# Kernel tuning notes

Measured on AMD Instinct MI355X. Metric: run time of the kernel, lower is better.

The kernel has to match this reference:

```python
import jax, jax.numpy as jnp
import numpy as np
from functools import partial

# dims
BATCH, L, H = 1, 512, 2048
NH, HD = 64, 64            # num heads, head dim
INTER = NH * HD            # 4096
G, N = 4, 64               # n_groups, ssm state size
K = 4                      # conv kernel
CONV = INTER + 2 * G * N   # 4608
PROJ = INTER + CONV + NH   # z, xBC, dt
EPS = 1e-5


def rmsnorm(x, w, eps=EPS):
    xf = x.astype(jnp.float32)
    v = jnp.mean(xf * xf, axis=-1, keepdims=True)
    return (xf * jax.lax.rsqrt(v + eps)).astype(x.dtype) * w


def setup_inputs() -> dict:
    key = jax.random.key(0)
    ks = jax.random.split(key, 12)
    rn = lambda k, s, sc=1.0: sc * jax.random.normal(k, s, dtype=jnp.float32)
    return {
        "hidden_states": rn(ks[0], (BATCH, L, H)),
        "residual": rn(ks[1], (BATCH, L, H)),
        "norm_w": 1.0 + rn(ks[2], (H,), 0.02),
        "in_proj_w": rn(ks[3], (H, PROJ), 0.02),
        "conv_w": rn(ks[4], (CONV, K), 0.2),
        "conv_b": rn(ks[5], (CONV,), 0.02),
        "A_log": jnp.log(jax.random.uniform(ks[6], (NH,), minval=1.0, maxval=16.0)),
        "dt_bias": rn(ks[7], (NH,), 0.5),
        "D": rn(ks[8], (NH,), 0.5),
        "gn_w": 1.0 + rn(ks[9], (INTER,), 0.02),
        "out_proj_w": rn(ks[10], (INTER, H), 0.02),
    }


def reference(hidden_states, residual, norm_w, in_proj_w, conv_w, conv_b,
              A_log, dt_bias, D, gn_w, out_proj_w):
    B_ = hidden_states.shape[0]
    # fused add + RMSNorm (residual is not None path)
    x = hidden_states + residual
    new_residual = x
    hs = rmsnorm(x, norm_w)

    # in_proj: [B,L,H] -> [B,L,PROJ] split into z | xBC | dt
    proj = jnp.einsum('blh,hp->blp', hs, in_proj_w)
    z = proj[..., :INTER]
    xBC = proj[..., INTER:INTER + CONV]
    dt = proj[..., INTER + CONV:]

    # causal depthwise conv of width K, then SiLU
    xp = jnp.pad(xBC, ((0, 0), (K - 1, 0), (0, 0)))
    conv = sum(xp[:, k:k + L, :] * conv_w[None, None, :, k] for k in range(K))
    xBC = jax.nn.silu(conv + conv_b)

    xh = xBC[..., :INTER].reshape(B_, L, NH, HD)
    Bm = xBC[..., INTER:INTER + G * N].reshape(B_, L, G, N)
    Cm = xBC[..., INTER + G * N:].reshape(B_, L, G, N)

    dt = jax.nn.softplus(dt + dt_bias)          # [B,L,NH]
    A = -jnp.exp(A_log)                         # [NH]
    dA = jnp.exp(dt * A)                        # [B,L,NH]

    hpg = NH // G
    Bh = jnp.repeat(Bm, hpg, axis=2)            # [B,L,NH,N]
    Ch = jnp.repeat(Cm, hpg, axis=2)

    def step(h, inp):
        dA_t, dt_t, x_t, B_t, C_t = inp
        # h: [B,NH,HD,N]
        h = h * dA_t[:, :, None, None] + (dt_t[:, :, None] * x_t)[..., None] * B_t[:, :, None, :]
        y = jnp.einsum('bhdn,bhn->bhd', h, C_t)
        return h, y

    h0 = jnp.zeros((B_, NH, HD, N), dtype=jnp.float32)
    xs = (jnp.moveaxis(dA, 1, 0), jnp.moveaxis(dt, 1, 0), jnp.moveaxis(xh, 1, 0),
          jnp.moveaxis(Bh, 1, 0), jnp.moveaxis(Ch, 1, 0))
    _, ys = jax.lax.scan(step, h0, xs)          # [L,B,NH,HD]
    y = jnp.moveaxis(ys, 0, 1) + xh * D[None, None, :, None]
    y = y.reshape(B_, L, INTER)

    # gated RMSNorm then out_proj
    y = rmsnorm(y * jax.nn.silu(z), gn_w)
    out = jnp.einsum('bli,ih->blh', y, out_proj_w)
    return out, new_residual
```

## Files before the change

kernel.cpp:

```cpp
#include <hip/hip_runtime.h>
#include <stdint.h>

#define LSEQ 512
#define HDIM 2048
#define NH 64
#define HD 64
#define INTER 4096
#define NG 4
#define NSTATE 64
#define CONVC 4608
#define PROJC 8768
#define EPS 1e-5f
#define CL 64
#define NC 8
#define NHDN (NH * HD * NSTATE)

typedef __attribute__((ext_vector_type(8))) short bf16x8;
typedef __attribute__((ext_vector_type(4))) short short4v;
typedef __attribute__((ext_vector_type(4))) float f32x4;

__device__ __forceinline__ short f2bf(float f) {
  union { float f; uint32_t u; } v; v.f = f;
  uint32_t r = v.u + 0x7FFFu + ((v.u >> 16) & 1u);
  return (short)(r >> 16);
}

__device__ __forceinline__ uint32_t cvt_pk_bf16(float lo, float hi) {
  uint32_t r;
  asm("v_cvt_pk_bf16_f32 %0, %1, %2" : "=v"(r) : "v"(lo), "v"(hi));
  return r;
}

__device__ __forceinline__ float bf2f(short s) {
  union { uint32_t u; float f; } v; v.u = ((uint32_t)(uint16_t)s) << 16;
  return v.f;
}

__device__ __forceinline__ float siluf(float v) {
  return v / (1.f + expf(-v));
}

__device__ __forceinline__ int xcd_swizzle(int orig, int nwg) {
  int q = nwg >> 3, r = nwg & 7;
  int xcd = orig & 7, idx = orig >> 3;
  return (xcd < r ? xcd * (q + 1) : r * (q + 1) + (xcd - r) * q) + idx;
}

__global__ __launch_bounds__(256) void k_add_rmsnorm(
    const float* __restrict__ hid, const float* __restrict__ res,
    const float* __restrict__ w, float* __restrict__ resid_out,
    short* __restrict__ hsb) {
  __shared__ float sred[4];
  const int row = blockIdx.x, tid = threadIdx.x;
  const float4* h4 = (const float4*)(hid + (size_t)row * HDIM);
  const float4* r4 = (const float4*)(res + (size_t)row * HDIM);
  float4* ro4 = (float4*)(resid_out + (size_t)row * HDIM);
  float4 a0 = h4[tid], b0 = r4[tid];
  float4 a1 = h4[tid + 256], b1 = r4[tid + 256];
  float4 xa, xb;
  xa.x = a0.x + b0.x; xa.y = a0.y + b0.y; xa.z = a0.z + b0.z; xa.w = a0.w + b0.w;
  xb.x = a1.x + b1.x; xb.y = a1.y + b1.y; xb.z = a1.z + b1.z; xb.w = a1.w + b1.w;
  ro4[tid] = xa; ro4[tid + 256] = xb;
  float ss = xa.x*xa.x + xa.y*xa.y + xa.z*xa.z + xa.w*xa.w
           + xb.x*xb.x + xb.y*xb.y + xb.z*xb.z + xb.w*xb.w;
  #pragma unroll
  for (int off = 32; off >= 1; off >>= 1) ss += __shfl_down(ss, off);
  if ((tid & 63) == 0) sred[tid >> 6] = ss;
  __syncthreads();
  float tot = sred[0] + sred[1] + sred[2] + sred[3];
  float rs = rsqrtf(tot / (float)HDIM + EPS);
  int e0 = tid * 4, e1 = (tid + 256) * 4;
  short4v s0, s1;
  s0.x = f2bf(xa.x * rs * w[e0+0]); s0.y = f2bf(xa.y * rs * w[e0+1]);
  s0.z = f2bf(xa.z * rs * w[e0+2]); s0.w = f2bf(xa.w * rs * w[e0+3]);
  s1.x = f2bf(xb.x * rs * w[e1+0]); s1.y = f2bf(xb.y * rs * w[e1+1]);
  s1.z = f2bf(xb.z * rs * w[e1+2]); s1.w = f2bf(xb.w * rs * w[e1+3]);
  *(short4v*)(hsb + (size_t)row * HDIM + e0) = s0;
  *(short4v*)(hsb + (size_t)row * HDIM + e1) = s1;
}

__global__ __launch_bounds__(256) void k_gemm1(
    const short* __restrict__ A, const float* __restrict__ Bw,
    short* __restrict__ zbf, short* __restrict__ xbc,
    float* __restrict__ dtf,
    const float* __restrict__ w2src, short* __restrict__ w2dst) {
  constexpr int BM = 128, MR = 4, WROWS = 64;
  const int M = LSEQ, N = PROJC, K = HDIM;
  __shared__ short lA[2][BM * 64];
  __shared__ short lB[64 * 64];
  const int tid = threadIdx.x, lane = tid & 63, wid = tid >> 6;

  const int NMB = M / BM, NNB = N / 64;
  const int nwg = NMB * NNB;

  if (blockIdx.x >= nwg) {
    float (*tile)[33] = (float(*)[33])lA;
    const int tb = blockIdx.x - nwg;
    const int tx = tid & 31, ty = tid >> 5;
    for (int i = 0; i < 16; ++i) {
      int t = tb + i * 512;
      int c0 = (t & 63) * 32;
      int r0 = (t >> 6) * 32;
      #pragma unroll
      for (int j = 0; j < 4; ++j)
        tile[ty + j*8][tx] = w2src[(size_t)(r0 + ty + j*8) * HDIM + c0 + tx];
      __syncthreads();
      #pragma unroll
      for (int j = 0; j < 4; ++j)
        w2dst[(size_t)(c0 + ty + j*8) * INTER + r0 + tx] = f2bf(tile[tx][ty + j*8]);
      __syncthreads();
    }
    return;
  }

  int wg = xcd_swizzle(blockIdx.x, nwg);
  const int mi = wg % NMB;
  const int ni = wg / NMB;
  const int m0 = mi * BM, n0 = ni * 64;
  const int wm = wid >> 1, wn = wid & 1;

  const int lrow8 = lane >> 3;
  const int cswz = ((lane & 7) ^ lrow8) * 8;

  auto stageA = [&](int buf, int kt) {
    #pragma unroll
    for (int r2 = 0; r2 < MR; ++r2) {
      int idx = r2 * 4 + wid;
      __builtin_amdgcn_global_load_lds(
          (const __attribute__((address_space(1))) int*)(A + (size_t)(m0 + idx * 8 + lrow8) * K + kt + cswz),
          (__attribute__((address_space(3))) int*)(&lA[buf][idx * 512]),
          16, 0, 0);
    }
  };

  float breg[16];
  auto loadB = [&](int kt) {
    #pragma unroll
    for (int r = 0; r < 2; ++r)
      #pragma unroll
      for (int j = 0; j < 8; ++j)
        breg[r * 8 + j] = Bw[(size_t)(kt + wid * 16 + r * 8 + j) * N + n0 + lane];
  };
  auto writeB = [&]() {
    #pragma unroll
    for (int r = 0; r < 2; ++r) {
      uint4 v;
      v.x = cvt_pk_bf16(breg[r*8+0], breg[r*8+1]);
      v.y = cvt_pk_bf16(breg[r*8+2], breg[r*8+3]);
      v.z = cvt_pk_bf16(breg[r*8+4], breg[r*8+5]);
      v.w = cvt_pk_bf16(breg[r*8+6], breg[r*8+7]);
      int ko = wid * 2 + r;
      *(uint4*)&lB[lane * 64 + ((ko ^ (lane & 7)) << 3)] = v;
    }
  };

  f32x4 acc[MR][2] = {};
  const int lrow = lane & 15, lkb = (lane >> 4) * 8;
  const int NT = K >> 6;
  loadB(0);
  stageA(0, 0);
  writeB();
  asm volatile("s_waitcnt vmcnt(0)" ::: "memory");
  asm volatile("s_waitcnt lgkmcnt(0)" ::: "memory");
  __builtin_amdgcn_s_barrier();
  for (int t = 0; t < NT; ++t) {
    int cur = t & 1;
    if (t + 1 < NT) {
      loadB((t + 1) * 64);
      stageA(cur ^ 1, (t + 1) * 64);
    }
    #pragma unroll
    for (int kk = 0; kk < 2; ++kk) {
      bf16x8 a[MR], b[2];
      #pragma unroll
      for (int m = 0; m < MR; ++m) {
        int row = wm * WROWS + m * 16 + lrow;
        int colel = (kk * 32 + lkb) ^ ((row & 7) << 3);
        a[m] = *(const bf16x8*)&lA[cur][row * 64 + colel];
      }
      #pragma unroll
      for (int n = 0; n < 2; ++n) {
        int row = wn * 32 + n * 16 + lrow;
        int colel = (kk * 32 + lkb) ^ ((row & 7) << 3);
        b[n] = *(const bf16x8*)&lB[row * 64 + colel];
      }
      #pragma unroll
      for (int m = 0; m < MR; ++m)
        #pragma unroll
        for (int n = 0; n < 2; ++n)
          acc[m][n] = __builtin_amdgcn_mfma_f32_16x16x32_bf16(a[m], b[n], acc[m][n], 0, 0, 0);
    }
    __builtin_amdgcn_s_barrier();
    if (t + 1 < NT) writeB();
    asm volatile("s_waitcnt vmcnt(0)" ::: "memory");
    asm volatile("s_waitcnt lgkmcnt(0)" ::: "memory");
    __builtin_amdgcn_s_barrier();
  }
  #pragma unroll
  for (int m = 0; m < MR; ++m) {
    int row = m0 + wm * WROWS + m * 16 + (lane >> 4) * 4;
    #pragma unroll
    for (int n = 0; n < 2; ++n) {
      int coll = wn * 32 + n * 16 + (lane & 15);
      #pragma unroll
      for (int r = 0; r < 4; ++r) {
        float v = acc[m][n][r];
        if (ni < 64)
          zbf[(size_t)(row + r) * INTER + n0 + coll] = f2bf(v);
        else if (ni < 136)
          xbc[(size_t)(row + r) * CONVC + (n0 - INTER) + coll] = f2bf(v);
        else
          dtf[(row + r) * 64 + coll] = v;
      }
    }
  }
}

template <int BM, int KS>
__global__ __launch_bounds__(256) void k_gemm_bf16(
    const short* __restrict__ A, const short* __restrict__ B,
    short* __restrict__ C, int M, int N, int K) {
  __shared__ short lA[2][BM * 64];
  __shared__ short lB[2][64 * 64];
  const int tid = threadIdx.x;
  const int lane = tid & 63, wid = tid >> 6;
  constexpr int MR = BM / 32;
  constexpr int WROWS = BM / 2;

  const int NMB = M / BM, NNB = N / 64;
  const int nwg = NMB * NNB * KS;
  int wg = xcd_swizzle(blockIdx.x, nwg);
  const int mi = wg % NMB;
  int rest = wg / NMB;
  const int zi = (KS > 1) ? (rest % KS) : 0;
  const int ni = (KS > 1) ? (rest / KS) : rest;
  const int m0 = mi * BM, n0 = ni * 64;
  const int wm = wid >> 1, wn = wid & 1;

  const int lrow8 = lane >> 3;
  const int cswz = ((lane & 7) ^ lrow8) * 8;

  const int Kc = K / KS;
  const int kbase = zi * Kc;
  short* Cp = C + (size_t)zi * M * N;

  auto stage = [&](int buf, int kt) {
    #pragma unroll
    for (int r2 = 0; r2 < MR; ++r2) {
      int idx = r2 * 4 + wid;
      __builtin_amdgcn_global_load_lds(
          (const __attribute__((address_space(1))) int*)(A + (size_t)(m0 + idx * 8 + lrow8) * K + kt + cswz),
          (__attribute__((address_space(3))) int*)(&lA[buf][idx * 512]),
          16, 0, 0);
    }
    #pragma unroll
    for (int r2 = 0; r2 < 2; ++r2) {
      int idx = r2 * 4 + wid;
      __builtin_amdgcn_global_load_lds(
          (const __attribute__((address_space(1))) int*)(B + (size_t)(n0 + idx * 8 + lrow8) * K + kt + cswz),
          (__attribute__((address_space(3))) int*)(&lB[buf][idx * 512]),
          16, 0, 0);
    }
  };

  f32x4 acc[MR][2] = {};
  const int lrow = lane & 15, lkb = (lane >> 4) * 8;
  const int NT = Kc >> 6;
  stage(0, kbase);
  for (int t = 0; t < NT; ++t) {
    int cur = t & 1;
    if (t + 1 < NT) {
      stage(cur ^ 1, kbase + (t + 1) * 64);
      if constexpr (MR == 2) asm volatile("s_waitcnt vmcnt(4)" ::: "memory");
      else                   asm volatile("s_waitcnt vmcnt(6)" ::: "memory");
    } else {
      asm volatile("s_waitcnt vmcnt(0)" ::: "memory");
    }
    __builtin_amdgcn_s_barrier();
    #pragma unroll
    for (int kk = 0; kk < 2; ++kk) {
      bf16x8 a[MR], b[2];
      #pragma unroll
      for (int m = 0; m < MR; ++m) {
        int row = wm * WROWS + m * 16 + lrow;
        int colel = (kk * 32 + lkb) ^ ((row & 7) << 3);
        a[m] = *(const bf16x8*)&lA[cur][row * 64 + colel];
      }
      #pragma unroll
      for (int n = 0; n < 2; ++n) {
        int row = wn * 32 + n * 16 + lrow;
        int colel = (kk * 32 + lkb) ^ ((row & 7) << 3);
        b[n] = *(const bf16x8*)&lB[cur][row * 64 + colel];
      }
      #pragma unroll
      for (int m = 0; m < MR; ++m)
        #pragma unroll
        for (int n = 0; n < 2; ++n)
          acc[m][n] = __builtin_amdgcn_mfma_f32_16x16x32_bf16(a[m], b[n], acc[m][n], 0, 0, 0);
    }
    __builtin_amdgcn_s_barrier();
  }
  #pragma unroll
  for (int m = 0; m < MR; ++m) {
    int row = m0 + wm * WROWS + m * 16 + (lane >> 4) * 4;
    int col = n0 + wn * 32 + (lane & 15);
    #pragma unroll
    for (int n = 0; n < 2; ++n)
      #pragma unroll
      for (int r = 0; r < 4; ++r)
        Cp[(size_t)(row + r) * N + col + n * 16] = f2bf(acc[m][n][r]);
  }
}

__global__ __launch_bounds__(256) void k_reduce4(
    const short* __restrict__ p, float* __restrict__ out, int n) {
  int i = (blockIdx.x * 256 + threadIdx.x) * 4;
  float4 o = {0.f, 0.f, 0.f, 0.f};
  #pragma unroll
  for (int z = 0; z < 4; ++z) {
    short4v v = *(const short4v*)(p + (size_t)z * n + i);
    o.x += bf2f(v.x); o.y += bf2f(v.y); o.z += bf2f(v.z); o.w += bf2f(v.w);
  }
  *(float4*)(out + i) = o;
}

__global__ __launch_bounds__(256) void k_conv(
    const short* __restrict__ xbc, const float* __restrict__ dtf,
    const float* __restrict__ cw, const float* __restrict__ cb,
    const float* __restrict__ A_log, const float* __restrict__ dt_bias,
    short* __restrict__ convo, float* __restrict__ dtb,
    float* __restrict__ ldab) {
  const int l0 = blockIdx.y * 64;
  if (blockIdx.x == CONVC / 256) {
    #pragma unroll
    for (int i = 0; i < 16; ++i) {
      int idx = threadIdx.x + i * 256;
      int l = l0 + (idx >> 6), h = idx & 63;
      float v = dtf[l * 64 + h] + dt_bias[h];
      float dt = v > 20.f ? v : log1pf(expf(v));
      float lda = dt * (-expf(A_log[h]));
      dtb[h * LSEQ + l] = dt;
      ldab[h * LSEQ + l] = lda;
    }
    return;
  }
  const int c = blockIdx.x * 256 + threadIdx.x;
  const float w0 = cw[c*4+0], w1 = cw[c*4+1], w2 = cw[c*4+2], w3 = cw[c*4+3];
  const float bias = cb[c];
  float x0 = 0.f, x1 = 0.f, x2 = 0.f;
  if (l0 > 0) {
    x0 = bf2f(xbc[(size_t)(l0-3) * CONVC + c]);
    x1 = bf2f(xbc[(size_t)(l0-2) * CONVC + c]);
    x2 = bf2f(xbc[(size_t)(l0-1) * CONVC + c]);
  }
  for (int l = l0; l < l0 + 64; ++l) {
    float x3 = bf2f(xbc[(size_t)l * CONVC + c]);
    float accv = bias + x0*w0 + x1*w1 + x2*w2 + x3*w3;
    convo[(size_t)l * CONVC + c] = f2bf(siluf(accv));
    x0 = x1; x1 = x2; x2 = x3;
  }
}

__global__ __launch_bounds__(256) void k_ssd(
    const short* __restrict__ convo, const float* __restrict__ dtb,
    const float* __restrict__ ldab, const float* __restrict__ Dp,
    short* __restrict__ ybuf, float* __restrict__ hend,
    float* __restrict__ Pbuf, float* __restrict__ cdbuf) {
  __shared__ __align__(16) short Xt[64 * 72];
  __shared__ __align__(16) short Bs[64 * 72];
  __shared__ __align__(16) short Cs[64 * 72];
  __shared__ __align__(16) short Btw[64 * 72];
  __shared__ __align__(16) short Ms[64 * 72];
  __shared__ float s_s[64], s_dt[64], s_w[64];
  const int c = blockIdx.x, head = blockIdx.y;
  const int g = head >> 4;
  const int tid = threadIdx.x, lane = tid & 63, wid = tid >> 6;
  const int l0 = c * CL;
  const short* xbase = convo + (size_t)l0 * CONVC + head * HD;
  const short* Bbase = convo + (size_t)l0 * CONVC + INTER + g * NSTATE;
  const short* Cbase = convo + (size_t)l0 * CONVC + INTER + NG * NSTATE + g * NSTATE;

  if (tid < 64) {
    float ps = ldab[head * LSEQ + l0 + tid];
    #pragma unroll
    for (int o = 1; o < 64; o <<= 1) {
      float u = __shfl_up(ps, o);
      if (tid >= o) ps += u;
    }
    float dtv = dtb[head * LSEQ + l0 + tid];
    s_s[tid] = ps;
    s_dt[tid] = dtv;
    float s63 = __shfl(ps, 63);
    s_w[tid] = __expf(s63 - ps) * dtv;
    cdbuf[head * LSEQ + l0 + tid] = __expf(ps);
    if (tid == 63) Pbuf[c * NH + head] = __expf(ps);
  }
  #pragma unroll
  for (int rep = 0; rep < 4; ++rep) {
    int l = (tid >> 4) + rep * 16;
    int d = (tid & 15) * 4;
    size_t roff = (size_t)l * CONVC;
    short4v xv = *(const short4v*)(xbase + roff + d);
    Xt[(d + 0) * 72 + l] = xv.x;
    Xt[(d + 1) * 72 + l] = xv.y;
    Xt[(d + 2) * 72 + l] = xv.z;
    Xt[(d + 3) * 72 + l] = xv.w;
    *(short4v*)&Bs[l * 72 + d] = *(const short4v*)(Bbase + roff + d);
    *(short4v*)&Cs[l * 72 + d] = *(const short4v*)(Cbase + roff + d);
  }
  __syncthreads();
  #pragma unroll
  for (int rep = 0; rep < 16; ++rep) {
    int idx = rep * 256 + tid;
    int l = idx >> 6, n = idx & 63;
    Btw[n * 72 + l] = f2bf(bf2f(Bs[l * 72 + n]) * s_w[l]);
  }
  __syncthreads();
  const int lrow = lane & 15, lkb = (lane >> 4) * 8;
  f32x4 sacc[4] = {};
  f32x4 hacc[4] = {};
  #pragma unroll
  for (int kk = 0; kk < 2; ++kk) {
    bf16x8 ac = *(const bf16x8*)&Cs[(wid * 16 + lrow) * 72 + kk * 32 + lkb];
    bf16x8 ax = *(const bf16x8*)&Xt[(wid * 16 + lrow) * 72 + kk * 32 + lkb];
    #pragma unroll
    for (int t4 = 0; t4 < 4; ++t4) {
      bf16x8 bb = *(const bf16x8*)&Bs[(t4 * 16 + lrow) * 72 + kk * 32 + lkb];
      bf16x8 bw = *(const bf16x8*)&Btw[(t4 * 16 + lrow) * 72 + kk * 32 + lkb];
      sacc[t4] = __builtin_amdgcn_mfma_f32_16x16x32_bf16(ac, bb, sacc[t4], 0, 0, 0);
      hacc[t4] = __builtin_amdgcn_mfma_f32_16x16x32_bf16(ax, bw, hacc[t4], 0, 0, 0);
    }
  }
  float* hb = hend + ((size_t)c * NH + head) * (HD * NSTATE);
  #pragma unroll
  for (int t4 = 0; t4 < 4; ++t4) {
    int j = t4 * 16 + lrow;
    float sj = s_s[j], dtj = s_dt[j];
    #pragma unroll
    for (int r = 0; r < 4; ++r) {
      int i = wid * 16 + (lane >> 4) * 4 + r;
      float m = (j <= i) ? __expf(s_s[i] - sj) * dtj * sacc[t4][r] : 0.f;
      Ms[i * 72 + j] = f2bf(m);
      hb[i * NSTATE + j] = hacc[t4][r];
    }
  }
  __syncthreads();
  f32x4 yacc[4] = {};
  #pragma unroll
  for (int kk = 0; kk < 2; ++kk) {
    bf16x8 am = *(const bf16x8*)&Ms[(wid * 16 + lrow) * 72 + kk * 32 + lkb];
    #pragma unroll
    for (int t4 = 0; t4 < 4; ++t4) {
      bf16x8 bx = *(const bf16x8*)&Xt[(t4 * 16 + lrow) * 72 + kk * 32 + lkb];
      yacc[t4] = __builtin_amdgcn_mfma_f32_16x16x32_bf16(am, bx, yacc[t4], 0, 0, 0);
    }
  }
  const float Dv = Dp[head];
  #pragma unroll
  for (int t4 = 0; t4 < 4; ++t4) {
    int d = t4 * 16 + lrow;
    #pragma unroll
    for (int r = 0; r < 4; ++r) {
      int i = wid * 16 + (lane >> 4) * 4 + r;
      float xv = bf2f(Xt[d * 72 + i]);
      ybuf[(size_t)(l0 + i) * INTER + head * HD + d] = f2bf(yacc[t4][r] + xv * Dv);
    }
  }
}

__global__ __launch_bounds__(256) void k_scan_combine(
    const float* __restrict__ hend, const float* __restrict__ Pbuf,
    float* __restrict__ hinbuf) {
  const int e = blockIdx.x * 256 + threadIdx.x;
  const int head = e >> 12;
  float h = 0.f;
  #pragma unroll
  for (int c = 1; c < NC; ++c) {
    h = Pbuf[(c - 1) * NH + head] * h + hend[(size_t)(c - 1) * NHDN + e];
    hinbuf[(size_t)c * NHDN + e] = h;
  }
}

__global__ __launch_bounds__(256) void k_scan_fixup(
    const short* __restrict__ convo, const float* __restrict__ hinbuf,
    const float* __restrict__ cdbuf, short* __restrict__ ybuf) {
  __shared__ float sh[NSTATE][HD + 1];
  __shared__ float sc[CL][NSTATE];
  __shared__ float scd[CL];
  const int bid = blockIdx.x;
  const int c = (bid >> 6) + 1, head = bid & 63, g = head >> 4;
  const int t = threadIdx.x;
  #pragma unroll
  for (int i = 0; i < 16; ++i) {
    int idx = t + i * 256;
    int d = idx >> 6, n = idx & 63;
    sh[n][d] = hinbuf[(size_t)c * NHDN + head * (HD * NSTATE) + idx];
  }
  #pragma unroll
  for (int i = 0; i < 16; ++i) {
    int idx = t + i * 256;
    int ll = idx >> 6, n = idx & 63;
    sc[ll][n] = bf2f(convo[(size_t)(c * CL + ll) * CONVC + INTER + NG * NSTATE + g * NSTATE + n]);
  }
  if (t < CL) scd[t] = cdbuf[head * LSEQ + c * CL + t];
  __syncthreads();
  const int d = t & 63, w = t >> 6;
  #pragma unroll
  for (int i = 0; i < 4; ++i) {
    int l0 = i * 16 + w * 4;
    float a0 = 0.f, a1 = 0.f, a2 = 0.f, a3 = 0.f;
    for (int n = 0; n < NSTATE; ++n) {
      float hv = sh[n][d];
      a0 += hv * sc[l0 + 0][n];
      a1 += hv * sc[l0 + 1][n];
      a2 += hv * sc[l0 + 2][n];
      a3 += hv * sc[l0 + 3][n];
    }
    size_t base = (size_t)(c * CL + l0) * INTER + head * HD + d;
    ybuf[base + 0 * INTER] = f2bf(bf2f(ybuf[base + 0 * INTER]) + scd[l0 + 0] * a0);
    ybuf[base + 1 * INTER] = f2bf(bf2f(ybuf[base + 1 * INTER]) + scd[l0 + 1] * a1);
    ybuf[base + 2 * INTER] = f2bf(bf2f(ybuf[base + 2 * INTER]) + scd[l0 + 2] * a2);
    ybuf[base + 3 * INTER] = f2bf(bf2f(ybuf[base + 3 * INTER]) + scd[l0 + 3] * a3);
  }
}

__global__ __launch_bounds__(256) void k_gated_norm(
    const short* __restrict__ ybuf, const short* __restrict__ zbf,
    const float* __restrict__ gw, short* __restrict__ y2b) {
  __shared__ float sred[4];
  const int row = blockIdx.x, tid = threadIdx.x;
  const short4v* y4 = (const short4v*)(ybuf + (size_t)row * INTER);
  const short4v* z4 = (const short4v*)(zbf + (size_t)row * INTER);
  float g[16];
  float ss = 0.f;
  #pragma unroll
  for (int i = 0; i < 4; ++i) {
    short4v y = y4[tid + i * 256];
    short4v z = z4[tid + i * 256];
    float g0 = bf2f(y.x) * siluf(bf2f(z.x)), g1 = bf2f(y.y) * siluf(bf2f(z.y));
    float g2 = bf2f(y.z) * siluf(bf2f(z.z)), g3 = bf2f(y.w) * siluf(bf2f(z.w));
    g[i*4+0] = g0; g[i*4+1] = g1; g[i*4+2] = g2; g[i*4+3] = g3;
    ss += g0*g0 + g1*g1 + g2*g2 + g3*g3;
  }
  #pragma unroll
  for (int off = 32; off >= 1; off >>= 1) ss += __shfl_down(ss, off);
  if ((tid & 63) == 0) sred[tid >> 6] = ss;
  __syncthreads();
  float tot = sred[0] + sred[1] + sred[2] + sred[3];
  float rs = rsqrtf(tot / (float)INTER + EPS);
  #pragma unroll
  for (int i = 0; i < 4; ++i) {
    int e = (tid + i * 256) * 4;
    short4v s;
    s.x = f2bf(g[i*4+0] * rs * gw[e+0]);
    s.y = f2bf(g[i*4+1] * rs * gw[e+1]);
    s.z = f2bf(g[i*4+2] * rs * gw[e+2]);
    s.w = f2bf(g[i*4+3] * rs * gw[e+3]);
    *(short4v*)(y2b + (size_t)row * INTER + e) = s;
  }
}

extern "C" void kernel_launch(void* const* d_in, const int* in_sizes, int n_in,
                              void* d_out, int out_size, void* d_ws, size_t ws_size,
                              hipStream_t stream) {
  const float* hid     = (const float*)d_in[0];
  const float* res     = (const float*)d_in[1];
  const float* norm_w  = (const float*)d_in[2];
  const float* w1      = (const float*)d_in[3];
  const float* cw      = (const float*)d_in[4];
  const float* cb      = (const float*)d_in[5];
  const float* A_log   = (const float*)d_in[6];
  const float* dt_bias = (const float*)d_in[7];
  const float* Dp      = (const float*)d_in[8];
  const float* gw      = (const float*)d_in[9];
  const float* w2      = (const float*)d_in[10];

  float* out = (float*)d_out;
  float* resid_out = out + (size_t)LSEQ * HDIM;

  char* ws = (char*)d_ws;
  short* hsb  = (short*)(ws);
  float* hend   = (float*)(ws + 2097152);
  short* p2     = (short*)(ws + 2097152);
  float* hinbuf = (float*)(ws + 10485760);
  float* Pbuf   = (float*)(ws + 18874368);
  float* cdbuf  = (float*)(ws + 18876416);
  short* zbf  = (short*)(ws + 38010880);
  short* xbc  = (short*)(ws + 42205184);
  float* dtf  = (float*)(ws + 46923776);
  short* convo= (short*)(ws + 55967744);
  float* dtb  = (float*)(ws + 65404928);
  float* ldab = (float*)(ws + 65536000);
  short* ybuf = (short*)(ws + 65667072);
  short* y2b  = (short*)(ws + 74055680);
  short* w2t  = (short*)(ws + 78249984);

  k_add_rmsnorm<<<LSEQ, 256, 0, stream>>>(hid, res, norm_w, resid_out, hsb);
  k_gemm1<<<(LSEQ/128)*(PROJC/64) + 512, 256, 0, stream>>>(hsb, w1, zbf, xbc, dtf, w2, w2t);
  k_conv<<<dim3(CONVC/256 + 1, NC), 256, 0, stream>>>(xbc, dtf, cw, cb, A_log, dt_bias, convo, dtb, ldab);
  k_ssd<<<dim3(NC, NH), 256, 0, stream>>>(convo, dtb, ldab, Dp, ybuf, hend, Pbuf, cdbuf);
  k_scan_combine<<<NHDN/256, 256, 0, stream>>>(hend, Pbuf, hinbuf);
  k_scan_fixup<<<(NC-1)*NH, 256, 0, stream>>>(convo, hinbuf, cdbuf, ybuf);
  k_gated_norm<<<LSEQ, 256, 0, stream>>>(ybuf, zbf, gw, y2b);
  k_gemm_bf16<64, 4><<<(LSEQ/64)*(HDIM/64)*4, 256, 0, stream>>>(y2b, w2t, p2, LSEQ, HDIM, INTER);
  k_reduce4<<<LSEQ*HDIM/1024, 256, 0, stream>>>(p2, out, LSEQ*HDIM);
}
```

Baseline: 120.7 us.

## Fuse x-channel causal conv and SiLU into SSD kernel, keep conv kernel for B/C only

The depthwise causal conv and SiLU for the 4096 x channels now run inside k_ssd while it loads each chunk tile, reading the raw in_proj output directly. k_conv handles only the 512 B/C channels plus the dt preprocessing, and writes them to a compact 512-wide buffer. This avoids writing and re-reading the full conv output for x and shrinks k_conv's grid. In exchange, k_ssd reads each x row four times (three halo rows) and does the conv math and extra global loads before its first sync.

```diff
diff --git a/kernel.cpp b/kernel.cpp
--- a/kernel.cpp
+++ b/kernel.cpp
@@ -14,6 +14,7 @@
 #define CL 64
 #define NC 8
 #define NHDN (NH * HD * NSTATE)
+#define BCC 512
 
 typedef __attribute__((ext_vector_type(8))) short bf16x8;
 typedef __attribute__((ext_vector_type(4))) short short4v;
@@ -328,10 +329,10 @@
     const short* __restrict__ xbc, const float* __restrict__ dtf,
     const float* __restrict__ cw, const float* __restrict__ cb,
     const float* __restrict__ A_log, const float* __restrict__ dt_bias,
-    short* __restrict__ convo, float* __restrict__ dtb,
+    short* __restrict__ convo2, float* __restrict__ dtb,
     float* __restrict__ ldab) {
   const int l0 = blockIdx.y * 64;
-  if (blockIdx.x == CONVC / 256) {
+  if (blockIdx.x == 2) {
     #pragma unroll
     for (int i = 0; i < 16; ++i) {
       int idx = threadIdx.x + i * 256;
@@ -345,25 +346,28 @@
     return;
   }
   const int c = blockIdx.x * 256 + threadIdx.x;
-  const float w0 = cw[c*4+0], w1 = cw[c*4+1], w2 = cw[c*4+2], w3 = cw[c*4+3];
-  const float bias = cb[c];
+  const int gc = INTER + c;
+  const float w0 = cw[gc*4+0], w1 = cw[gc*4+1], w2 = cw[gc*4+2], w3 = cw[gc*4+3];
+  const float bias = cb[gc];
   float x0 = 0.f, x1 = 0.f, x2 = 0.f;
   if (l0 > 0) {
-    x0 = bf2f(xbc[(size_t)(l0-3) * CONVC + c]);
-    x1 = bf2f(xbc[(size_t)(l0-2) * CONVC + c]);
-    x2 = bf2f(xbc[(size_t)(l0-1) * CONVC + c]);
+    x0 = bf2f(xbc[(size_t)(l0-3) * CONVC + gc]);
+    x1 = bf2f(xbc[(size_t)(l0-2) * CONVC + gc]);
+    x2 = bf2f(xbc[(size_t)(l0-1) * CONVC + gc]);
   }
   for (int l = l0; l < l0 + 64; ++l) {
-    float x3 = bf2f(xbc[(size_t)l * CONVC + c]);
+    float x3 = bf2f(xbc[(size_t)l * CONVC + gc]);
     float accv = bias + x0*w0 + x1*w1 + x2*w2 + x3*w3;
-    convo[(size_t)l * CONVC + c] = f2bf(siluf(accv));
+    convo2[(size_t)l * BCC + c] = f2bf(siluf(accv));
     x0 = x1; x1 = x2; x2 = x3;
   }
 }
 
 __global__ __launch_bounds__(256) void k_ssd(
-    const short* __restrict__ convo, const float* __restrict__ dtb,
-    const float* __restrict__ ldab, const float* __restrict__ Dp,
+    const short* __restrict__ xbc, const short* __restrict__ convo2,
+    const float* __restrict__ cw, const float* __restrict__ cb,
+    const float* __restrict__ dtb, const float* __restrict__ ldab,
+    const float* __restrict__ Dp,
     short* __restrict__ ybuf, float* __restrict__ hend,
     float* __restrict__ Pbuf, float* __restrict__ cdbuf) {
   __shared__ __align__(16) short Xt[64 * 72];
@@ -376,9 +380,8 @@
   const int g = head >> 4;
   const int tid = threadIdx.x, lane = tid & 63, wid = tid >> 6;
   const int l0 = c * CL;
-  const short* xbase = convo + (size_t)l0 * CONVC + head * HD;
-  const short* Bbase = convo + (size_t)l0 * CONVC + INTER + g * NSTATE;
-  const short* Cbase = convo + (size_t)l0 * CONVC + INTER + NG * NSTATE + g * NSTATE;
+  const short* Bbase = convo2 + (size_t)l0 * BCC + g * NSTATE;
+  const short* Cbase = convo2 + (size_t)l0 * BCC + 256 + g * NSTATE;
 
   if (tid < 64) {
     float ps = ldab[head * LSEQ + l0 + tid];
@@ -395,18 +398,40 @@
     cdbuf[head * LSEQ + l0 + tid] = __expf(ps);
     if (tid == 63) Pbuf[c * NH + head] = __expf(ps);
   }
+  const int dch = (tid & 15) * 4;
+  const int ch = head * HD + dch;
+  float cwv[4][4], cbv[4];
+  #pragma unroll
+  for (int i = 0; i < 4; ++i) {
+    float4 w4 = *(const float4*)(cw + (size_t)(ch + i) * 4);
+    cwv[i][0] = w4.x; cwv[i][1] = w4.y; cwv[i][2] = w4.z; cwv[i][3] = w4.w;
+    cbv[i] = cb[ch + i];
+  }
   #pragma unroll
   for (int rep = 0; rep < 4; ++rep) {
     int l = (tid >> 4) + rep * 16;
-    int d = (tid & 15) * 4;
-    size_t roff = (size_t)l * CONVC;
-    short4v xv = *(const short4v*)(xbase + roff + d);
-    Xt[(d + 0) * 72 + l] = xv.x;
-    Xt[(d + 1) * 72 + l] = xv.y;
-    Xt[(d + 2) * 72 + l] = xv.z;
-    Xt[(d + 3) * 72 + l] = xv.w;
-    *(short4v*)&Bs[l * 72 + d] = *(const short4v*)(Bbase + roff + d);
-    *(short4v*)&Cs[l * 72 + d] = *(const short4v*)(Cbase + roff + d);
+    int gl = l0 + l;
+    float xr[4][4];
+    #pragma unroll
+    for (int k = 0; k < 4; ++k) {
+      int r = gl - 3 + k;
+      if (r >= 0) {
+        short4v v = *(const short4v*)(xbc + (size_t)r * CONVC + ch);
+        xr[k][0] = bf2f(v.x); xr[k][1] = bf2f(v.y);
+        xr[k][2] = bf2f(v.z); xr[k][3] = bf2f(v.w);
+      } else {
+        xr[k][0] = xr[k][1] = xr[k][2] = xr[k][3] = 0.f;
+      }
+    }
+    #pragma unroll
+    for (int i = 0; i < 4; ++i) {
+      float a = cbv[i] + xr[0][i]*cwv[i][0] + xr[1][i]*cwv[i][1]
+                       + xr[2][i]*cwv[i][2] + xr[3][i]*cwv[i][3];
+      Xt[(dch + i) * 72 + l] = f2bf(siluf(a));
+    }
+    size_t roff = (size_t)l * BCC;
+    *(short4v*)&Bs[l * 72 + dch] = *(const short4v*)(Bbase + roff + dch);
+    *(short4v*)&Cs[l * 72 + dch] = *(const short4v*)(Cbase + roff + dch);
   }
   __syncthreads();
   #pragma unroll
@@ -482,7 +507,7 @@
 }
 
 __global__ __launch_bounds__(256) void k_scan_fixup(
-    const short* __restrict__ convo, const float* __restrict__ hinbuf,
+    const short* __restrict__ convo2, const float* __restrict__ hinbuf,
     const float* __restrict__ cdbuf, short* __restrict__ ybuf) {
   __shared__ float sh[NSTATE][HD + 1];
   __shared__ float sc[CL][NSTATE];
@@ -500,7 +525,7 @@
   for (int i = 0; i < 16; ++i) {
     int idx = t + i * 256;
     int ll = idx >> 6, n = idx & 63;
-    sc[ll][n] = bf2f(convo[(size_t)(c * CL + ll) * CONVC + INTER + NG * NSTATE + g * NSTATE + n]);
+    sc[ll][n] = bf2f(convo2[(size_t)(c * CL + ll) * BCC + 256 + g * NSTATE + n]);
   }
   if (t < CL) scd[t] = cdbuf[head * LSEQ + c * CL + t];
   __syncthreads();
@@ -588,7 +613,7 @@
   short* zbf  = (short*)(ws + 38010880);
   short* xbc  = (short*)(ws + 42205184);
   float* dtf  = (float*)(ws + 46923776);
-  short* convo= (short*)(ws + 55967744);
+  short* convo2 = (short*)(ws + 55967744);
   float* dtb  = (float*)(ws + 65404928);
   float* ldab = (float*)(ws + 65536000);
   short* ybuf = (short*)(ws + 65667072);
@@ -597,10 +622,10 @@
 
   k_add_rmsnorm<<<LSEQ, 256, 0, stream>>>(hid, res, norm_w, resid_out, hsb);
   k_gemm1<<<(LSEQ/128)*(PROJC/64) + 512, 256, 0, stream>>>(hsb, w1, zbf, xbc, dtf, w2, w2t);
-  k_conv<<<dim3(CONVC/256 + 1, NC), 256, 0, stream>>>(xbc, dtf, cw, cb, A_log, dt_bias, convo, dtb, ldab);
-  k_ssd<<<dim3(NC, NH), 256, 0, stream>>>(convo, dtb, ldab, Dp, ybuf, hend, Pbuf, cdbuf);
+  k_conv<<<dim3(3, NC), 256, 0, stream>>>(xbc, dtf, cw, cb, A_log, dt_bias, convo2, dtb, ldab);
+  k_ssd<<<dim3(NC, NH), 256, 0, stream>>>(xbc, convo2, cw, cb, dtb, ldab, Dp, ybuf, hend, Pbuf, cdbuf);
   k_scan_combine<<<NHDN/256, 256, 0, stream>>>(hend, Pbuf, hinbuf);
-  k_scan_fixup<<<(NC-1)*NH, 256, 0, stream>>>(convo, hinbuf, cdbuf, ybuf);
+  k_scan_fixup<<<(NC-1)*NH, 256, 0, stream>>>(convo2, hinbuf, cdbuf, ybuf);
   k_gated_norm<<<LSEQ, 256, 0, stream>>>(ybuf, zbf, gw, y2b);
   k_gemm_bf16<64, 4><<<(LSEQ/64)*(HDIM/64)*4, 256, 0, stream>>>(y2b, w2t, p2, LSEQ, HDIM, INTER);
   k_reduce4<<<LSEQ*HDIM/1024, 256, 0, stream>>>(p2, out, LSEQ*HDIM);
```

Result: slower. 126.2 us (+4.6%).
